# Kernel optimization log

Hardware: AMD Instinct MI355X
Metric: run time of the kernel (lower is better)

The kernel has to match this reference:

```python
import jax, jax.numpy as jnp
import numpy as np

B, L, D, H, DEPTH, K = 16, 2048, 256, 8, 2, 7
HD = D // H
SCALE = HD ** -0.5


def _ln(x, g, b, eps=1e-5):
    m = x.mean(-1, keepdims=True)
    v = ((x - m) ** 2).mean(-1, keepdims=True)
    return (x - m) * jax.lax.rsqrt(v + eps) * g + b


def _nat_attn(x, qkv_w, qkv_b, proj_w, proj_b):
    # Neighborhood attention 1D: window of K tokens centered on each token,
    # clamped at sequence edges (NATTEN semantics, dilation=1).
    b, l, d = x.shape
    qkv = (x @ qkv_w + qkv_b).reshape(b, l, 3, H, HD).transpose(2, 0, 3, 1, 4)  # [3,B,H,L,hd]
    q, k, v = qkv[0] * SCALE, qkv[1], qkv[2]
    starts = jnp.clip(jnp.arange(l) - K // 2, 0, l - K)          # [L]
    idx = starts[:, None] + jnp.arange(K)                        # [L,K]
    kn = k[:, :, idx]                                            # [B,H,L,K,hd]
    vn = v[:, :, idx]
    attn = jax.nn.softmax(jnp.einsum('bhld,bhlkd->bhlk', q, kn), axis=-1)
    out = jnp.einsum('bhlk,bhlkd->bhld', attn, vn)               # [B,H,L,hd]
    out = out.transpose(0, 2, 1, 3).reshape(b, l, d)
    return out @ proj_w + proj_b


def _mlp(x, w1, b1, w2, b2):
    return jax.nn.gelu(x @ w1 + b1, approximate=False) @ w2 + b2


def setup_inputs() -> dict:
    key = jax.random.key(0)
    ks = jax.random.split(key, 8)
    s = 0.02
    return {
        'x': jax.random.normal(ks[0], (B, L, D), jnp.float32),
        'ln1_g': jnp.ones((DEPTH, D), jnp.float32),
        'ln1_b': jnp.zeros((DEPTH, D), jnp.float32),
        'qkv_w': jax.random.normal(ks[1], (DEPTH, D, 3 * D), jnp.float32) * s,
        'qkv_b': jnp.zeros((DEPTH, 3 * D), jnp.float32),
        'proj_w': jax.random.normal(ks[2], (DEPTH, D, D), jnp.float32) * s,
        'proj_b': jnp.zeros((DEPTH, D), jnp.float32),
        'ln2_g': jnp.ones((DEPTH, D), jnp.float32),
        'ln2_b': jnp.zeros((DEPTH, D), jnp.float32),
        'fc1_w': jax.random.normal(ks[3], (DEPTH, D, 4 * D), jnp.float32) * s,
        'fc1_b': jnp.zeros((DEPTH, 4 * D), jnp.float32),
        'fc2_w': jax.random.normal(ks[4], (DEPTH, 4 * D, D), jnp.float32) * s,
        'fc2_b': jnp.zeros((DEPTH, D), jnp.float32),
        'conv_w': jax.random.normal(ks[5], (2 * D, D, 3), jnp.float32) * s,  # OIH
        'dn_g': jnp.ones((2 * D,), jnp.float32),
        'dn_b': jnp.zeros((2 * D,), jnp.float32),
    }


def reference(x, ln1_g, ln1_b, qkv_w, qkv_b, proj_w, proj_b,
              ln2_g, ln2_b, fc1_w, fc1_b, fc2_w, fc2_b,
              conv_w, dn_g, dn_b):
    for i in range(DEPTH):
        h = _nat_attn(_ln(x, ln1_g[i], ln1_b[i]), qkv_w[i], qkv_b[i], proj_w[i], proj_b[i])
        x = x + h
        x = x + _mlp(_ln(x, ln2_g[i], ln2_b[i]), fc1_w[i], fc1_b[i], fc2_w[i], fc2_b[i])
    # ConvDownsampler: Conv1d(D, 2D, k=3, s=2, p=1, bias=False) + LayerNorm
    xc = x.transpose(0, 2, 1)  # [B,C,L]
    y = jax.lax.conv_general_dilated(xc, conv_w, window_strides=(2,),
                                     padding=[(1, 1)],
                                     dimension_numbers=('NCH', 'OIH', 'NCH'))
    y = y.transpose(0, 2, 1)   # [B, L//2, 2D]
    y = _ln(y, dn_g, dn_b)
    return (y, x)
```

## Files before the change

kernel.cpp:

```cpp
#include <hip/hip_runtime.h>

typedef unsigned short u16;
typedef __attribute__((ext_vector_type(8))) short bf16x8;
typedef __attribute__((ext_vector_type(4))) float f32x4;

__device__ __forceinline__ float bf2f(u16 u) { return __uint_as_float(((unsigned)u) << 16); }
__device__ __forceinline__ u16 f2bf(float f) {
    unsigned u = __float_as_uint(f);
    return (u16)((u + 0x7FFFu + ((u >> 16) & 1u)) >> 16);
}

__device__ __forceinline__ void load_lds16(const u16* g, u16* l) {
    __builtin_amdgcn_global_load_lds(
        (const __attribute__((address_space(1))) unsigned int*)g,
        (__attribute__((address_space(3))) unsigned int*)l,
        16, 0, 0);
}

template<int EPI>
__global__ __launch_bounds__(256) void gemm_kernel(
    const u16* __restrict__ A, const u16* __restrict__ Wt,
    const float* __restrict__ bias, const float* __restrict__ res,
    void* __restrict__ outp, int M, int N, int K)
{
    __shared__ __align__(16) u16 As[128 * 32];
    __shared__ __align__(16) u16 Bs[128 * 32];
    const int tid  = threadIdx.x;
    const int lane = tid & 63;
    const int wave = tid >> 6;
    const int row0 = blockIdx.x * 128;
    const int col0 = blockIdx.y * 128;
    const int wr = (wave >> 1) * 64;
    const int wc = (wave & 1) * 64;
    const int lr = lane & 15;
    const int kq = (lane >> 4) * 8;

    f32x4 acc[4][4];
#pragma unroll
    for (int i = 0; i < 4; ++i)
#pragma unroll
        for (int j = 0; j < 4; ++j) acc[i][j] = (f32x4){0.f, 0.f, 0.f, 0.f};

    const int srow = tid >> 2;
    const int scol = (tid & 3) * 8;
    const u16* ag = A  + (size_t)(row0 + srow) * K + scol;
    const u16* bg = Wt + (size_t)(col0 + srow) * K + scol;
    const size_t rstep = (size_t)64 * K;
    u16* alp = As + tid * 8;
    u16* blp = Bs + tid * 8;

    for (int k0 = 0; k0 < K; k0 += 32) {
        __syncthreads();
        load_lds16(ag + k0,         alp);
        load_lds16(ag + rstep + k0, alp + 64 * 32);
        load_lds16(bg + k0,         blp);
        load_lds16(bg + rstep + k0, blp + 64 * 32);
        __syncthreads();
        bf16x8 af[4], bfv[4];
#pragma unroll
        for (int i = 0; i < 4; ++i) af[i]  = *(const bf16x8*)(As + (wr + i * 16 + lr) * 32 + kq);
#pragma unroll
        for (int j = 0; j < 4; ++j) bfv[j] = *(const bf16x8*)(Bs + (wc + j * 16 + lr) * 32 + kq);
#pragma unroll
        for (int i = 0; i < 4; ++i)
#pragma unroll
            for (int j = 0; j < 4; ++j)
                acc[i][j] = __builtin_amdgcn_mfma_f32_16x16x32_bf16(af[i], bfv[j], acc[i][j], 0, 0, 0);
    }

#pragma unroll
    for (int i = 0; i < 4; ++i) {
        const int rbase = row0 + wr + i * 16 + (lane >> 4) * 4;
#pragma unroll
        for (int j = 0; j < 4; ++j) {
            const int col = col0 + wc + j * 16 + lr;
            const float bv = (EPI == 3) ? 0.f : bias[col];
#pragma unroll
            for (int r = 0; r < 4; ++r) {
                const int row = rbase + r;
                float v = acc[i][j][r] + bv;
                if (EPI == 1) {
                    v += res[(size_t)row * N + col];
                    ((float*)outp)[(size_t)row * N + col] = v;
                } else {
                    if (EPI == 2) v = 0.5f * v * (1.f + erff(v * 0.70710678118654752f));
                    ((u16*)outp)[(size_t)row * N + col] = f2bf(v);
                }
            }
        }
    }
}

__global__ __launch_bounds__(256) void ln_f2b_kernel(
    const float* __restrict__ x, const float* __restrict__ g,
    const float* __restrict__ be, u16* __restrict__ out)
{
    const int lane = threadIdx.x & 63;
    const int row  = blockIdx.x * 4 + (threadIdx.x >> 6);
    const float4 a = *(const float4*)(x + (size_t)row * 256 + lane * 4);
    float v[4] = {a.x, a.y, a.z, a.w};
    float s = v[0] + v[1] + v[2] + v[3];
#pragma unroll
    for (int m = 1; m < 64; m <<= 1) s += __shfl_xor(s, m);
    const float mean = s * (1.f / 256.f);
    float s2 = 0.f;
#pragma unroll
    for (int e = 0; e < 4; ++e) { float d = v[e] - mean; s2 += d * d; }
#pragma unroll
    for (int m = 1; m < 64; m <<= 1) s2 += __shfl_xor(s2, m);
    const float rstd = rsqrtf(s2 * (1.f / 256.f) + 1e-5f);
    const float4 gg = *(const float4*)(g + lane * 4);
    const float4 bb = *(const float4*)(be + lane * 4);
    ushort4 o;
    o.x = f2bf((v[0] - mean) * rstd * gg.x + bb.x);
    o.y = f2bf((v[1] - mean) * rstd * gg.y + bb.y);
    o.z = f2bf((v[2] - mean) * rstd * gg.z + bb.z);
    o.w = f2bf((v[3] - mean) * rstd * gg.w + bb.w);
    *(ushort4*)(out + (size_t)row * 256 + lane * 4) = o;
}

__global__ __launch_bounds__(256) void ln_b2f_kernel(
    const u16* __restrict__ x, const float* __restrict__ g,
    const float* __restrict__ be, float* __restrict__ out)
{
    const int lane = threadIdx.x & 63;
    const int row  = blockIdx.x * 4 + (threadIdx.x >> 6);
    const u16* xr = x + (size_t)row * 512 + lane * 8;
    float v[8];
#pragma unroll
    for (int e = 0; e < 8; e += 4) {
        ushort4 a = *(const ushort4*)(xr + e);
        v[e] = bf2f(a.x); v[e+1] = bf2f(a.y); v[e+2] = bf2f(a.z); v[e+3] = bf2f(a.w);
    }
    float s = 0.f;
#pragma unroll
    for (int e = 0; e < 8; ++e) s += v[e];
#pragma unroll
    for (int m = 1; m < 64; m <<= 1) s += __shfl_xor(s, m);
    const float mean = s * (1.f / 512.f);
    float s2 = 0.f;
#pragma unroll
    for (int e = 0; e < 8; ++e) { float d = v[e] - mean; s2 += d * d; }
#pragma unroll
    for (int m = 1; m < 64; m <<= 1) s2 += __shfl_xor(s2, m);
    const float rstd = rsqrtf(s2 * (1.f / 512.f) + 1e-5f);
    float* orow = out + (size_t)row * 512 + lane * 8;
#pragma unroll
    for (int e = 0; e < 8; e += 4) {
        float4 o;
        o.x = (v[e]   - mean) * rstd * g[lane*8+e]   + be[lane*8+e];
        o.y = (v[e+1] - mean) * rstd * g[lane*8+e+1] + be[lane*8+e+1];
        o.z = (v[e+2] - mean) * rstd * g[lane*8+e+2] + be[lane*8+e+2];
        o.w = (v[e+3] - mean) * rstd * g[lane*8+e+3] + be[lane*8+e+3];
        *(float4*)(orow + e) = o;
    }
}

__global__ __launch_bounds__(256) void attn_kernel(
    const u16* __restrict__ qkv, u16* __restrict__ out)
{
    const int lane  = threadIdx.x & 63;
    const int token = blockIdx.x * 4 + (threadIdx.x >> 6);
    const int b = token >> 11;
    const int l = token & 2047;
    const int h = lane >> 3;
    const int s = lane & 7;
    const int off = h * 32 + s * 4;

    ushort4 q4 = *(const ushort4*)(qkv + (size_t)token * 768 + off);
    const float scale = 0.17677669529663687f;
    float q0 = bf2f(q4.x), q1 = bf2f(q4.y), q2 = bf2f(q4.z), q3 = bf2f(q4.w);

    int start = l - 3;
    start = start < 0 ? 0 : (start > 2041 ? 2041 : start);
    const u16* kbase = qkv + ((size_t)(b << 11) + start) * 768 + 256 + off;

    float sc[7], vv[7][4];
#pragma unroll
    for (int j = 0; j < 7; ++j) {
        const u16* kp = kbase + (size_t)j * 768;
        ushort4 k4 = *(const ushort4*)kp;
        ushort4 v4 = *(const ushort4*)(kp + 256);
        float d = q0 * bf2f(k4.x) + q1 * bf2f(k4.y) + q2 * bf2f(k4.z) + q3 * bf2f(k4.w);
        d += __shfl_xor(d, 1); d += __shfl_xor(d, 2); d += __shfl_xor(d, 4);
        sc[j] = d * scale;
        vv[j][0] = bf2f(v4.x); vv[j][1] = bf2f(v4.y); vv[j][2] = bf2f(v4.z); vv[j][3] = bf2f(v4.w);
    }
    float mx = sc[0];
#pragma unroll
    for (int j = 1; j < 7; ++j) mx = fmaxf(mx, sc[j]);
    float p[7], sum = 0.f;
#pragma unroll
    for (int j = 0; j < 7; ++j) { p[j] = expf(sc[j] - mx); sum += p[j]; }
    const float inv = 1.f / sum;
    float o0 = 0, o1 = 0, o2 = 0, o3 = 0;
#pragma unroll
    for (int j = 0; j < 7; ++j) {
        o0 += p[j] * vv[j][0]; o1 += p[j] * vv[j][1];
        o2 += p[j] * vv[j][2]; o3 += p[j] * vv[j][3];
    }
    ushort4 o;
    o.x = f2bf(o0 * inv); o.y = f2bf(o1 * inv); o.z = f2bf(o2 * inv); o.w = f2bf(o3 * inv);
    *(ushort4*)(out + (size_t)token * 256 + off) = o;
}

__global__ void transpose_kernel(const float* __restrict__ in, u16* __restrict__ out,
                                 int K, int N, int total)
{
    int idx = blockIdx.x * 256 + threadIdx.x;
    if (idx >= total) return;
    int k = idx % K;
    int n = (idx / K) % N;
    int d = idx / (K * N);
    out[idx] = f2bf(in[(size_t)d * K * N + (size_t)k * N + n]);
}

__global__ void convw_kernel(const float* __restrict__ in, u16* __restrict__ out)
{
    int idx = blockIdx.x * 256 + threadIdx.x;
    int r  = idx % 768;
    int co = idx / 768;
    int t  = r / 256;
    int ci = r % 256;
    out[idx] = f2bf(in[(size_t)co * 768 + (size_t)ci * 3 + t]);
}

__global__ __launch_bounds__(256) void im2col_kernel(
    const float* __restrict__ x, u16* __restrict__ x2, int r0)
{
    int idx = blockIdx.x * 256 + threadIdx.x;
    int c4  = idx & 63;
    int t   = (idx >> 6) % 3;
    int rl  = idx / 192;
    int row = r0 + rl;
    int b   = row >> 10;
    int lo  = row & 1023;
    int l   = 2 * lo + t - 1;
    ushort4 o = {0, 0, 0, 0};
    if (l >= 0 && l < 2048) {
        float4 val = *(const float4*)(x + ((size_t)(b << 11) + l) * 256 + c4 * 4);
        o.x = f2bf(val.x); o.y = f2bf(val.y); o.z = f2bf(val.z); o.w = f2bf(val.w);
    }
    *(ushort4*)(x2 + (size_t)rl * 768 + t * 256 + c4 * 4) = o;
}

extern "C" void kernel_launch(void* const* d_in, const int* in_sizes, int n_in,
                              void* d_out, int out_size, void* d_ws, size_t ws_size,
                              hipStream_t stream)
{
    const float* x_in   = (const float*)d_in[0];
    const float* ln1_g  = (const float*)d_in[1];
    const float* ln1_b  = (const float*)d_in[2];
    const float* qkv_w  = (const float*)d_in[3];
    const float* qkv_b  = (const float*)d_in[4];
    const float* proj_w = (const float*)d_in[5];
    const float* proj_b = (const float*)d_in[6];
    const float* ln2_g  = (const float*)d_in[7];
    const float* ln2_b  = (const float*)d_in[8];
    const float* fc1_w  = (const float*)d_in[9];
    const float* fc1_b  = (const float*)d_in[10];
    const float* fc2_w  = (const float*)d_in[11];
    const float* fc2_b  = (const float*)d_in[12];
    const float* conv_w = (const float*)d_in[13];
    const float* dn_g   = (const float*)d_in[14];
    const float* dn_b   = (const float*)d_in[15];

    float* xbuf = (float*)d_out + 8388608;
    u16*   xn   = (u16*)d_out;

    char* ws = (char*)d_ws;
    const size_t MB = 1024ull * 1024;
    u16* qkv_wt  = (u16*)ws;
    u16* proj_wt = qkv_wt  + 2 * 768 * 256;
    u16* fc1_wt  = proj_wt + 2 * 256 * 256;
    u16* fc2_wt  = fc1_wt  + 2 * 1024 * 256;
    u16* conv_wt = fc2_wt  + 2 * 256 * 1024;
    u16* S       = (u16*)(ws + 4 * MB);

    const size_t R = ws_size > 4 * MB ? ws_size - 4 * MB : 0;
    int nb = 16;    while (nb > 1 && (size_t)nb * 4 * MB > R) nb >>= 1;
    int Mf = 32768; while (Mf > 2048 && (size_t)Mf * 2048 > R) Mf >>= 1;
    int Mc = 16384; while (Mc > 2048 && (size_t)Mc * 2560 > R) Mc >>= 1;

    transpose_kernel<<<(2*256*768 + 255) / 256, 256, 0, stream>>>(qkv_w,  qkv_wt,  256, 768, 2*256*768);
    transpose_kernel<<<(2*256*256 + 255) / 256, 256, 0, stream>>>(proj_w, proj_wt, 256, 256, 2*256*256);
    transpose_kernel<<<(2*256*1024 + 255) / 256, 256, 0, stream>>>(fc1_w, fc1_wt,  256, 1024, 2*256*1024);
    transpose_kernel<<<(2*1024*256 + 255) / 256, 256, 0, stream>>>(fc2_w, fc2_wt,  1024, 256, 2*1024*256);
    convw_kernel<<<(512*768) / 256, 256, 0, stream>>>(conv_w, conv_wt);

    hipMemcpyAsync(xbuf, x_in, 32768ull * 256 * 4, hipMemcpyDeviceToDevice, stream);

    for (int layer = 0; layer < 2; ++layer) {
        const float* l1g = ln1_g + layer * 256;
        const float* l1b = ln1_b + layer * 256;
        const float* l2g = ln2_g + layer * 256;
        const float* l2b = ln2_b + layer * 256;
        const u16*   qwt = qkv_wt  + (size_t)layer * 768 * 256;
        const float* qb  = qkv_b   + layer * 768;
        const u16*   pwt = proj_wt + (size_t)layer * 256 * 256;
        const float* pb  = proj_b  + layer * 256;
        const u16*   f1w = fc1_wt  + (size_t)layer * 1024 * 256;
        const float* f1b = fc1_b   + layer * 1024;
        const u16*   f2w = fc2_wt  + (size_t)layer * 256 * 1024;
        const float* f2b = fc2_b   + layer * 256;

        ln_f2b_kernel<<<8192, 256, 0, stream>>>(xbuf, l1g, l1b, xn);
        {
            const int Mg = nb * 2048;
            u16* qkvc  = S;
            u16* atnoc = S + (size_t)Mg * 768;
            for (int g = 0; g < 16 / nb; ++g) {
                const size_t t0 = (size_t)g * Mg;
                gemm_kernel<0><<<dim3(Mg / 128, 6), 256, 0, stream>>>(
                    xn + t0 * 256, qwt, qb, nullptr, qkvc, Mg, 768, 256);
                attn_kernel<<<Mg / 4, 256, 0, stream>>>(qkvc, atnoc);
                gemm_kernel<1><<<dim3(Mg / 128, 2), 256, 0, stream>>>(
                    atnoc, pwt, pb, xbuf + t0 * 256, xbuf + t0 * 256, Mg, 256, 256);
            }
        }
        ln_f2b_kernel<<<8192, 256, 0, stream>>>(xbuf, l2g, l2b, xn);
        {
            u16* hbuf = S;
            for (int q = 0; q < 32768 / Mf; ++q) {
                const size_t r0 = (size_t)q * Mf;
                gemm_kernel<2><<<dim3(Mf / 128, 8), 256, 0, stream>>>(
                    xn + r0 * 256, f1w, f1b, nullptr, hbuf, Mf, 1024, 256);
                gemm_kernel<1><<<dim3(Mf / 128, 2), 256, 0, stream>>>(
                    hbuf, f2w, f2b, xbuf + r0 * 256, xbuf + r0 * 256, Mf, 256, 1024);
            }
        }
    }

    {
        u16* x2c = S;
        u16* ycc = S + (size_t)Mc * 768;
        for (int c = 0; c < 16384 / Mc; ++c) {
            const int r0 = c * Mc;
            im2col_kernel<<<3 * Mc / 4, 256, 0, stream>>>(xbuf, x2c, r0);
            gemm_kernel<3><<<dim3(Mc / 128, 4), 256, 0, stream>>>(
                x2c, conv_wt, nullptr, nullptr, ycc, Mc, 512, 768);
            ln_b2f_kernel<<<Mc / 4, 256, 0, stream>>>(
                ycc, dn_g, dn_b, (float*)d_out + (size_t)r0 * 512);
        }
    }
}
```

Before: 503.5 us.

## Double-buffer GEMM LDS tiles and stage bf16 epilogue through LDS for vector stores

The GEMM main loop now ping-pongs between two LDS buffers. The next K-slice is issued via global_load_lds before computing on the current one, and one barrier per iteration replaces two. For bf16-output epilogues, results are first written into a padded LDS tile in two column halves, then copied to global memory with 16-byte vector stores instead of scattered 2-byte stores. This doubles LDS use per block, which may reduce occupancy, and adds extra barriers in the epilogue.

```diff
diff --git a/kernel.cpp b/kernel.cpp
--- a/kernel.cpp
+++ b/kernel.cpp
@@ -23,8 +23,7 @@
     const float* __restrict__ bias, const float* __restrict__ res,
     void* __restrict__ outp, int M, int N, int K)
 {
-    __shared__ __align__(16) u16 As[128 * 32];
-    __shared__ __align__(16) u16 Bs[128 * 32];
+    __shared__ __align__(16) u16 POOL[4 * 128 * 32];
     const int tid  = threadIdx.x;
     const int lane = tid & 63;
     const int wave = tid >> 6;
@@ -46,21 +45,36 @@
     const u16* ag = A  + (size_t)(row0 + srow) * K + scol;
     const u16* bg = Wt + (size_t)(col0 + srow) * K + scol;
     const size_t rstep = (size_t)64 * K;
-    u16* alp = As + tid * 8;
-    u16* blp = Bs + tid * 8;
-
-    for (int k0 = 0; k0 < K; k0 += 32) {
+
+    {
+        u16* Ac = POOL;
+        u16* Bc = POOL + 128 * 32;
+        load_lds16(ag,         Ac + tid * 8);
+        load_lds16(ag + rstep, Ac + 64 * 32 + tid * 8);
+        load_lds16(bg,         Bc + tid * 8);
+        load_lds16(bg + rstep, Bc + 64 * 32 + tid * 8);
+    }
+
+    const int niter = K >> 5;
+    for (int it = 0; it < niter; ++it) {
+        const int cur = it & 1;
+        u16* Ac = POOL + cur * 2 * 128 * 32;
+        u16* Bc = Ac + 128 * 32;
         __syncthreads();
-        load_lds16(ag + k0,         alp);
-        load_lds16(ag + rstep + k0, alp + 64 * 32);
-        load_lds16(bg + k0,         blp);
-        load_lds16(bg + rstep + k0, blp + 64 * 32);
-        __syncthreads();
+        if (it + 1 < niter) {
+            const int k0 = (it + 1) << 5;
+            u16* An = POOL + (cur ^ 1) * 2 * 128 * 32;
+            u16* Bn = An + 128 * 32;
+            load_lds16(ag + k0,         An + tid * 8);
+            load_lds16(ag + rstep + k0, An + 64 * 32 + tid * 8);
+            load_lds16(bg + k0,         Bn + tid * 8);
+            load_lds16(bg + rstep + k0, Bn + 64 * 32 + tid * 8);
+        }
         bf16x8 af[4], bfv[4];
 #pragma unroll
-        for (int i = 0; i < 4; ++i) af[i]  = *(const bf16x8*)(As + (wr + i * 16 + lr) * 32 + kq);
-#pragma unroll
-        for (int j = 0; j < 4; ++j) bfv[j] = *(const bf16x8*)(Bs + (wc + j * 16 + lr) * 32 + kq);
+        for (int i = 0; i < 4; ++i) af[i]  = *(const bf16x8*)(Ac + (wr + i * 16 + lr) * 32 + kq);
+#pragma unroll
+        for (int j = 0; j < 4; ++j) bfv[j] = *(const bf16x8*)(Bc + (wc + j * 16 + lr) * 32 + kq);
 #pragma unroll
         for (int i = 0; i < 4; ++i)
 #pragma unroll
@@ -68,25 +82,52 @@
                 acc[i][j] = __builtin_amdgcn_mfma_f32_16x16x32_bf16(af[i], bfv[j], acc[i][j], 0, 0, 0);
     }
 
-#pragma unroll
-    for (int i = 0; i < 4; ++i) {
-        const int rbase = row0 + wr + i * 16 + (lane >> 4) * 4;
-#pragma unroll
-        for (int j = 0; j < 4; ++j) {
-            const int col = col0 + wc + j * 16 + lr;
-            const float bv = (EPI == 3) ? 0.f : bias[col];
-#pragma unroll
-            for (int r = 0; r < 4; ++r) {
-                const int row = rbase + r;
-                float v = acc[i][j][r] + bv;
-                if (EPI == 1) {
-                    v += res[(size_t)row * N + col];
+    if (EPI == 1) {
+#pragma unroll
+        for (int i = 0; i < 4; ++i) {
+            const int rbase = row0 + wr + i * 16 + (lane >> 4) * 4;
+#pragma unroll
+            for (int j = 0; j < 4; ++j) {
+                const int col = col0 + wc + j * 16 + lr;
+                const float bv = bias[col];
+#pragma unroll
+                for (int r = 0; r < 4; ++r) {
+                    const int row = rbase + r;
+                    float v = acc[i][j][r] + bv + res[(size_t)row * N + col];
                     ((float*)outp)[(size_t)row * N + col] = v;
-                } else {
-                    if (EPI == 2) v = 0.5f * v * (1.f + erff(v * 0.70710678118654752f));
-                    ((u16*)outp)[(size_t)row * N + col] = f2bf(v);
                 }
             }
+        }
+    } else {
+        constexpr int ES = 80;
+        u16* Es = POOL;
+        for (int p = 0; p < 2; ++p) {
+            __syncthreads();
+            if ((wave & 1) == p) {
+#pragma unroll
+                for (int i = 0; i < 4; ++i) {
+                    const int rl = wr + i * 16 + (lane >> 4) * 4;
+#pragma unroll
+                    for (int j = 0; j < 4; ++j) {
+                        const int cl = j * 16 + lr;
+                        const float bv = (EPI == 3) ? 0.f : bias[col0 + p * 64 + cl];
+#pragma unroll
+                        for (int r = 0; r < 4; ++r) {
+                            float v = acc[i][j][r] + bv;
+                            if (EPI == 2) v = 0.5f * v * (1.f + erff(v * 0.70710678118654752f));
+                            Es[(rl + r) * ES + cl] = f2bf(v);
+                        }
+                    }
+                }
+            }
+            __syncthreads();
+            const int row = tid >> 1;
+            const int ch  = (tid & 1) * 32;
+            const u16* src = Es + row * ES + ch;
+            u16* dst = (u16*)outp + (size_t)(row0 + row) * N + col0 + p * 64 + ch;
+#pragma unroll
+            for (int e = 0; e < 4; ++e)
+                *(uint4*)(dst + e * 8) = *(const uint4*)(src + e * 8);
         }
     }
 }
```

Measured after the change: 574.9 us. +14.2%, slower.

## Stage full-K swizzled weight panels in LDS and read activations directly

Applied to the files above, without the earlier changes.

The GEMM kernel is restructured. Each block now loads a whole 128-column by 256-K weight panel into LDS (64KB), using a new pre-swizzled weight layout produced by new prep kernels. Activations are read straight from global memory into MFMA fragments rather than staged through LDS. This removes the per-32-K double barrier loop, but the uncoalesced global A loads and the large LDS footprint can lower occupancy and load efficiency.

```diff
diff --git a/kernel.cpp b/kernel.cpp
--- a/kernel.cpp
+++ b/kernel.cpp
@@ -17,23 +17,22 @@
         16, 0, 0);
 }
 
-template<int EPI>
-__global__ __launch_bounds__(256) void gemm_kernel(
-    const u16* __restrict__ A, const u16* __restrict__ Wt,
+template<int K, int EPI>
+__global__ __launch_bounds__(256) void gemm2_kernel(
+    const u16* __restrict__ A, const u16* __restrict__ Wsw,
     const float* __restrict__ bias, const float* __restrict__ res,
-    void* __restrict__ outp, int M, int N, int K)
-{
-    __shared__ __align__(16) u16 As[128 * 32];
-    __shared__ __align__(16) u16 Bs[128 * 32];
+    void* __restrict__ outp, int M, int N)
+{
+    __shared__ __align__(16) u16 Bs[128 * 256];
     const int tid  = threadIdx.x;
     const int lane = tid & 63;
     const int wave = tid >> 6;
     const int row0 = blockIdx.x * 128;
-    const int col0 = blockIdx.y * 128;
+    const int pan  = blockIdx.y;
     const int wr = (wave >> 1) * 64;
     const int wc = (wave & 1) * 64;
     const int lr = lane & 15;
-    const int kq = (lane >> 4) * 8;
+    const int kq = lane >> 4;
 
     f32x4 acc[4][4];
 #pragma unroll
@@ -41,39 +40,42 @@
 #pragma unroll
         for (int j = 0; j < 4; ++j) acc[i][j] = (f32x4){0.f, 0.f, 0.f, 0.f};
 
-    const int srow = tid >> 2;
-    const int scol = (tid & 3) * 8;
-    const u16* ag = A  + (size_t)(row0 + srow) * K + scol;
-    const u16* bg = Wt + (size_t)(col0 + srow) * K + scol;
-    const size_t rstep = (size_t)64 * K;
-    u16* alp = As + tid * 8;
-    u16* blp = Bs + tid * 8;
-
-    for (int k0 = 0; k0 < K; k0 += 32) {
+    const u16* wbase = Wsw + (size_t)pan * K * 128;
+
+    for (int ko = 0; ko < K; ko += 256) {
+        if (ko) __syncthreads();
+        const u16* src = wbase + (size_t)ko * 128;
+#pragma unroll
+        for (int p = 0; p < 16; ++p)
+            load_lds16(src + p * 2048 + tid * 8, Bs + p * 2048 + tid * 8);
         __syncthreads();
-        load_lds16(ag + k0,         alp);
-        load_lds16(ag + rstep + k0, alp + 64 * 32);
-        load_lds16(bg + k0,         blp);
-        load_lds16(bg + rstep + k0, blp + 64 * 32);
-        __syncthreads();
-        bf16x8 af[4], bfv[4];
-#pragma unroll
-        for (int i = 0; i < 4; ++i) af[i]  = *(const bf16x8*)(As + (wr + i * 16 + lr) * 32 + kq);
-#pragma unroll
-        for (int j = 0; j < 4; ++j) bfv[j] = *(const bf16x8*)(Bs + (wc + j * 16 + lr) * 32 + kq);
-#pragma unroll
-        for (int i = 0; i < 4; ++i)
+
+#pragma unroll
+        for (int kk = 0; kk < 8; ++kk) {
+            const int kglob = ko + kk * 32 + kq * 8;
+            bf16x8 af[4];
+#pragma unroll
+            for (int i = 0; i < 4; ++i)
+                af[i] = *(const bf16x8*)(A + (size_t)(row0 + wr + i * 16 + lr) * K + kglob);
+            bf16x8 bfv[4];
 #pragma unroll
             for (int j = 0; j < 4; ++j)
-                acc[i][j] = __builtin_amdgcn_mfma_f32_16x16x32_bf16(af[i], bfv[j], acc[i][j], 0, 0, 0);
-    }
-
+                bfv[j] = *(const bf16x8*)(Bs + (size_t)((kk * 4 + kq) * 128 + wc + j * 16 + lr) * 8);
+#pragma unroll
+            for (int i = 0; i < 4; ++i)
+#pragma unroll
+                for (int j = 0; j < 4; ++j)
+                    acc[i][j] = __builtin_amdgcn_mfma_f32_16x16x32_bf16(af[i], bfv[j], acc[i][j], 0, 0, 0);
+        }
+    }
+
+    const int col00 = pan * 128;
 #pragma unroll
     for (int i = 0; i < 4; ++i) {
         const int rbase = row0 + wr + i * 16 + (lane >> 4) * 4;
 #pragma unroll
         for (int j = 0; j < 4; ++j) {
-            const int col = col0 + wc + j * 16 + lr;
+            const int col = col00 + wc + j * 16 + lr;
             const float bv = (EPI == 3) ? 0.f : bias[col];
 #pragma unroll
             for (int r = 0; r < 4; ++r) {
@@ -91,6 +93,44 @@
     }
 }
 
+__global__ void wswz_kernel(const float* __restrict__ in, u16* __restrict__ out,
+                            int K, int N, int total)
+{
+    int g = blockIdx.x * 256 + threadIdx.x;
+    if (g >= total) return;
+    int nl  = g & 127;
+    int t   = g >> 7;
+    int kqq = t % (K >> 3);
+    int dp  = t / (K >> 3);
+    int p   = dp % (N >> 7);
+    int d   = dp / (N >> 7);
+    int n_g = p * 128 + nl;
+    int k0  = kqq * 8;
+    const float* s = in + ((size_t)d * K + k0) * N + n_g;
+    u16 o[8];
+#pragma unroll
+    for (int e = 0; e < 8; ++e) o[e] = f2bf(s[(size_t)e * N]);
+    *(uint4*)(out + (size_t)g * 8) = *(const uint4*)o;
+}
+
+__global__ void cwswz_kernel(const float* __restrict__ in, u16* __restrict__ out)
+{
+    int g = blockIdx.x * 256 + threadIdx.x;
+    int nl  = g & 127;
+    int kqq = (g >> 7) % 96;
+    int p   = (g >> 7) / 96;
+    int co  = p * 128 + nl;
+    u16 o[8];
+#pragma unroll
+    for (int e = 0; e < 8; ++e) {
+        int k  = kqq * 8 + e;
+        int t  = k >> 8;
+        int ci = k & 255;
+        o[e] = f2bf(in[(size_t)co * 768 + ci * 3 + t]);
+    }
+    *(uint4*)(out + (size_t)g * 8) = *(const uint4*)o;
+}
+
 __global__ __launch_bounds__(256) void ln_f2b_kernel(
     const float* __restrict__ x, const float* __restrict__ g,
     const float* __restrict__ be, u16* __restrict__ out)
@@ -202,27 +242,6 @@
     ushort4 o;
     o.x = f2bf(o0 * inv); o.y = f2bf(o1 * inv); o.z = f2bf(o2 * inv); o.w = f2bf(o3 * inv);
     *(ushort4*)(out + (size_t)token * 256 + off) = o;
-}
-
-__global__ void transpose_kernel(const float* __restrict__ in, u16* __restrict__ out,
-                                 int K, int N, int total)
-{
-    int idx = blockIdx.x * 256 + threadIdx.x;
-    if (idx >= total) return;
-    int k = idx % K;
-    int n = (idx / K) % N;
-    int d = idx / (K * N);
-    out[idx] = f2bf(in[(size_t)d * K * N + (size_t)k * N + n]);
-}
-
-__global__ void convw_kernel(const float* __restrict__ in, u16* __restrict__ out)
-{
-    int idx = blockIdx.x * 256 + threadIdx.x;
-    int r  = idx % 768;
-    int co = idx / 768;
-    int t  = r / 256;
-    int ci = r % 256;
-    out[idx] = f2bf(in[(size_t)co * 768 + (size_t)ci * 3 + t]);
 }
 
 __global__ __launch_bounds__(256) void im2col_kernel(
@@ -282,11 +301,11 @@
     int Mf = 32768; while (Mf > 2048 && (size_t)Mf * 2048 > R) Mf >>= 1;
     int Mc = 16384; while (Mc > 2048 && (size_t)Mc * 2560 > R) Mc >>= 1;
 
-    transpose_kernel<<<(2*256*768 + 255) / 256, 256, 0, stream>>>(qkv_w,  qkv_wt,  256, 768, 2*256*768);
-    transpose_kernel<<<(2*256*256 + 255) / 256, 256, 0, stream>>>(proj_w, proj_wt, 256, 256, 2*256*256);
-    transpose_kernel<<<(2*256*1024 + 255) / 256, 256, 0, stream>>>(fc1_w, fc1_wt,  256, 1024, 2*256*1024);
-    transpose_kernel<<<(2*1024*256 + 255) / 256, 256, 0, stream>>>(fc2_w, fc2_wt,  1024, 256, 2*1024*256);
-    convw_kernel<<<(512*768) / 256, 256, 0, stream>>>(conv_w, conv_wt);
+    wswz_kernel<<<(2*256*768)  / 8 / 256, 256, 0, stream>>>(qkv_w,  qkv_wt,  256, 768,  2*256*768/8);
+    wswz_kernel<<<(2*256*256)  / 8 / 256, 256, 0, stream>>>(proj_w, proj_wt, 256, 256,  2*256*256/8);
+    wswz_kernel<<<(2*256*1024) / 8 / 256, 256, 0, stream>>>(fc1_w,  fc1_wt,  256, 1024, 2*256*1024/8);
+    wswz_kernel<<<(2*1024*256) / 8 / 256, 256, 0, stream>>>(fc2_w,  fc2_wt,  1024, 256, 2*1024*256/8);
+    cwswz_kernel<<<(512*768) / 8 / 256, 256, 0, stream>>>(conv_w, conv_wt);
 
     hipMemcpyAsync(xbuf, x_in, 32768ull * 256 * 4, hipMemcpyDeviceToDevice, stream);
 
@@ -311,11 +330,11 @@
             u16* atnoc = S + (size_t)Mg * 768;
             for (int g = 0; g < 16 / nb; ++g) {
                 const size_t t0 = (size_t)g * Mg;
-                gemm_kernel<0><<<dim3(Mg / 128, 6), 256, 0, stream>>>(
-                    xn + t0 * 256, qwt, qb, nullptr, qkvc, Mg, 768, 256);
+                gemm2_kernel<256, 0><<<dim3(Mg / 128, 6), 256, 0, stream>>>(
+                    xn + t0 * 256, qwt, qb, nullptr, qkvc, Mg, 768);
                 attn_kernel<<<Mg / 4, 256, 0, stream>>>(qkvc, atnoc);
-                gemm_kernel<1><<<dim3(Mg / 128, 2), 256, 0, stream>>>(
-                    atnoc, pwt, pb, xbuf + t0 * 256, xbuf + t0 * 256, Mg, 256, 256);
+                gemm2_kernel<256, 1><<<dim3(Mg / 128, 2), 256, 0, stream>>>(
+                    atnoc, pwt, pb, xbuf + t0 * 256, xbuf + t0 * 256, Mg, 256);
             }
         }
         ln_f2b_kernel<<<8192, 256, 0, stream>>>(xbuf, l2g, l2b, xn);
@@ -323,10 +342,10 @@
             u16* hbuf = S;
             for (int q = 0; q < 32768 / Mf; ++q) {
                 const size_t r0 = (size_t)q * Mf;
-                gemm_kernel<2><<<dim3(Mf / 128, 8), 256, 0, stream>>>(
-                    xn + r0 * 256, f1w, f1b, nullptr, hbuf, Mf, 1024, 256);
-                gemm_kernel<1><<<dim3(Mf / 128, 2), 256, 0, stream>>>(
-                    hbuf, f2w, f2b, xbuf + r0 * 256, xbuf + r0 * 256, Mf, 256, 1024);
+                gemm2_kernel<256, 2><<<dim3(Mf / 128, 8), 256, 0, stream>>>(
+                    xn + r0 * 256, f1w, f1b, nullptr, hbuf, Mf, 1024);
+                gemm2_kernel<1024, 1><<<dim3(Mf / 128, 2), 256, 0, stream>>>(
+                    hbuf, f2w, f2b, xbuf + r0 * 256, xbuf + r0 * 256, Mf, 256);
             }
         }
     }
@@ -337,8 +356,8 @@
         for (int c = 0; c < 16384 / Mc; ++c) {
             const int r0 = c * Mc;
             im2col_kernel<<<3 * Mc / 4, 256, 0, stream>>>(xbuf, x2c, r0);
-            gemm_kernel<3><<<dim3(Mc / 128, 4), 256, 0, stream>>>(
-                x2c, conv_wt, nullptr, nullptr, ycc, Mc, 512, 768);
+            gemm2_kernel<768, 3><<<dim3(Mc / 128, 4), 256, 0, stream>>>(
+                x2c, conv_wt, nullptr, nullptr, ycc, Mc, 512);
             ln_b2f_kernel<<<Mc / 4, 256, 0, stream>>>(
                 ycc, dn_g, dn_b, (float*)d_out + (size_t)r0 * 512);
         }
```

Result: slower. 568.0 us (+12.8%).
